# Optimization experiments

Hardware: AMD Instinct MI355X
Metric: run time of the kernel (lower is better)

The kernel has to match this reference:

```python
import jax, jax.numpy as jnp
import numpy as np

EMBED_DIM = 768
FF_DIM = 3072
NUM_EXPERTS = 8
TOP_K = 2
CAPACITY_FACTOR = 1.25  # training-mode capacity factor
LB_WEIGHT = 0.01
Z_WEIGHT = 0.001


def setup_inputs() -> dict:
    key = jax.random.key(0)
    k0, k1, k2, k3, k4 = jax.random.split(key, 5)
    B, S, D, F, E = 4, 2048, EMBED_DIM, FF_DIM, NUM_EXPERTS
    scale_d = 1.0 / np.sqrt(D)
    scale_f = 1.0 / np.sqrt(F)
    return {
        "x": jax.random.normal(k0, (B, S, D), dtype=jnp.float32),
        # router gate: nn.Linear(D, E, bias=False) -> weight [E, D]
        "w_gate": jax.random.normal(k1, (E, D), dtype=jnp.float32) * scale_d,
        # stacked expert weights, torch Linear layout [out, in]
        "wi_gate": jax.random.normal(k2, (E, F, D), dtype=jnp.float32) * scale_d,
        "wi_up": jax.random.normal(k3, (E, F, D), dtype=jnp.float32) * scale_d,
        "wo": jax.random.normal(k4, (E, D, F), dtype=jnp.float32) * scale_f,
    }


def moe_forward(x, w_gate, wi_gate, wi_up, wo):
    B, S, D = x.shape
    E = w_gate.shape[0]
    K = TOP_K
    T = B * S
    capacity = max(int(T * K / E * CAPACITY_FACTOR), K)

    xf = x.reshape(T, D)
    router_logits = xf @ w_gate.T                        # [T, E]
    router_probs = jax.nn.softmax(router_logits, axis=-1)
    topk_probs, topk_idx = jax.lax.top_k(router_probs, K)  # [T, K]
    topk_probs = topk_probs / topk_probs.sum(axis=-1, keepdims=True)

    # one-hot dispatch mask [T, K, E]
    onehot = (topk_idx[:, :, None] == jnp.arange(E)[None, None, :]).astype(xf.dtype)
    # per-(k, expert) arrival rank of each token (torch truncates first `capacity`
    # tokens in token-index order, independently per k and per expert)
    rank = ((jnp.cumsum(onehot, axis=0) - onehot) * onehot).sum(-1)  # [T, K]
    keep = (rank < capacity).astype(xf.dtype)                        # [T, K]

    # combine weights per (token, expert) [T, E]
    combine = jnp.einsum('tk,tk,tke->te', topk_probs, keep, onehot)

    out = jnp.zeros_like(xf)
    for e in range(E):  # fixed small structural loop over experts
        gate = jax.nn.silu(xf @ wi_gate[e].T)   # [T, F]
        up = xf @ wi_up[e].T                    # [T, F]
        y = (gate * up) @ wo[e].T               # [T, D]
        out = out + y * combine[:, e:e + 1]

    # auxiliary losses
    expert_mask = onehot.sum(axis=1)            # [T, E]
    f = expert_mask.sum(axis=0) / (T * K)
    P = router_probs.mean(axis=0)
    load_balance_loss = E * (f * P).sum()
    z_loss = jnp.mean(jax.nn.logsumexp(router_logits, axis=-1) ** 2)
    aux_loss = LB_WEIGHT * load_balance_loss + Z_WEIGHT * z_loss

    return out.reshape(B, S, D), aux_loss


def reference(x, w_gate, wi_gate, wi_up, wo):
    return moe_forward(x, w_gate, wi_gate, wi_up, wo)
```

## Files before the change

### kernel.cpp

```cpp
#include <hip/hip_runtime.h>

typedef unsigned short u16;
typedef unsigned int u32;
typedef unsigned long long u64;

#define T_TOK 8192
#define DIM 768
#define FF 3072
#define NE 8
#define CAP 2560
#define LSTR 5120
#define MAXMT 20

typedef __attribute__((ext_vector_type(8))) short s8v;
typedef __attribute__((ext_vector_type(4))) float f4v;

__device__ __forceinline__ u16 f2bf(float f) {
  union { float f; u32 u; } v; v.f = f;
  u32 r = v.u + 0x7FFFu + ((v.u >> 16) & 1u);
  return (u16)(r >> 16);
}

__device__ __forceinline__ void glds16(const void* g, void* l) {
  __builtin_amdgcn_global_load_lds(
      (const __attribute__((address_space(1))) u32*)g,
      (__attribute__((address_space(3))) u32*)l, 16, 0, 0);
}

__global__ void cast_bf16_kernel(const float* __restrict__ src, u16* __restrict__ dst, int n8) {
  int i = blockIdx.x * blockDim.x + threadIdx.x;
  if (i >= n8) return;
  const float4* s4 = (const float4*)src;
  float4 a = s4[2 * i], b = s4[2 * i + 1];
  uint4 o;
  o.x = (u32)f2bf(a.x) | ((u32)f2bf(a.y) << 16);
  o.y = (u32)f2bf(a.z) | ((u32)f2bf(a.w) << 16);
  o.z = (u32)f2bf(b.x) | ((u32)f2bf(b.y) << 16);
  o.w = (u32)f2bf(b.z) | ((u32)f2bf(b.w) << 16);
  ((uint4*)dst)[i] = o;
}

__global__ __launch_bounds__(256) void router_kernel(
    const float* __restrict__ x, const float* __restrict__ wg,
    int* __restrict__ tki, float* __restrict__ tkp,
    float* __restrict__ probs, float* __restrict__ lse2) {
  int lane = threadIdx.x & 63;
  int t = blockIdx.x * 4 + (threadIdx.x >> 6);
  const float* xr = x + (long)t * DIM;
  float acc[NE];
#pragma unroll
  for (int e = 0; e < NE; e++) acc[e] = 0.f;
  for (int i = 0; i < DIM / 64; i++) {
    float xv = xr[lane + 64 * i];
#pragma unroll
    for (int e = 0; e < NE; e++) acc[e] += xv * wg[e * DIM + lane + 64 * i];
  }
#pragma unroll
  for (int off = 32; off > 0; off >>= 1) {
#pragma unroll
    for (int e = 0; e < NE; e++) acc[e] += __shfl_xor(acc[e], off);
  }
  if (lane == 0) {
    float m = acc[0];
#pragma unroll
    for (int e = 1; e < NE; e++) m = fmaxf(m, acc[e]);
    float p[NE], s = 0.f;
#pragma unroll
    for (int e = 0; e < NE; e++) { p[e] = __expf(acc[e] - m); s += p[e]; }
    float inv = 1.f / s;
    int e0 = 0;
#pragma unroll
    for (int e = 1; e < NE; e++) if (acc[e] > acc[e0]) e0 = e;
    int e1 = (e0 == 0) ? 1 : 0;
#pragma unroll
    for (int e = 0; e < NE; e++) if (e != e0 && acc[e] > acc[e1]) e1 = e;
    float p0 = p[e0] * inv, p1 = p[e1] * inv;
    float rn = 1.f / (p0 + p1);
    tki[2 * t] = e0; tki[2 * t + 1] = e1;
    tkp[2 * t] = p0 * rn; tkp[2 * t + 1] = p1 * rn;
    float4 pa = {p[0] * inv, p[1] * inv, p[2] * inv, p[3] * inv};
    float4 pb = {p[4] * inv, p[5] * inv, p[6] * inv, p[7] * inv};
    ((float4*)(probs + t * 8))[0] = pa;
    ((float4*)(probs + t * 8))[1] = pb;
    float lse = __logf(s) + m;
    lse2[t] = lse * lse;
  }
}

__global__ __launch_bounds__(1024) void reduce_router_kernel(
    const int* __restrict__ tki, const float* __restrict__ probs, const float* __restrict__ lse2,
    int* __restrict__ fcnt, float* __restrict__ psum, float* __restrict__ zsum) {
  int t = blockIdx.x * 1024 + threadIdx.x;
  float4 pa = ((const float4*)(probs + t * 8))[0];
  float4 pb = ((const float4*)(probs + t * 8))[1];
  float p[8] = {pa.x, pa.y, pa.z, pa.w, pb.x, pb.y, pb.z, pb.w};
  float z = lse2[t];
  int e0 = tki[2 * t], e1 = tki[2 * t + 1];
  int fc[8];
#pragma unroll
  for (int e = 0; e < 8; e++) fc[e] = (e0 == e ? 1 : 0) + (e1 == e ? 1 : 0);
#pragma unroll
  for (int off = 32; off > 0; off >>= 1) {
#pragma unroll
    for (int e = 0; e < 8; e++) { p[e] += __shfl_xor(p[e], off); fc[e] += __shfl_xor(fc[e], off); }
    z += __shfl_xor(z, off);
  }
  __shared__ float sp[16][9];
  __shared__ int sf[16][8];
  int wv = threadIdx.x >> 6, lane = threadIdx.x & 63;
  if (lane == 0) {
#pragma unroll
    for (int e = 0; e < 8; e++) { sp[wv][e] = p[e]; sf[wv][e] = fc[e]; }
    sp[wv][8] = z;
  }
  __syncthreads();
  if (threadIdx.x < 9) {
    float s = 0.f;
    for (int w = 0; w < 16; w++) s += sp[w][threadIdx.x];
    if (threadIdx.x < 8) atomicAdd(&psum[threadIdx.x], s);
    else atomicAdd(zsum, s);
  }
  if (threadIdx.x >= 64 && threadIdx.x < 72) {
    int e = threadIdx.x - 64;
    int s = 0;
    for (int w = 0; w < 16; w++) s += sf[w][e];
    atomicAdd(&fcnt[e], s);
  }
}

__global__ __launch_bounds__(1024) void rank_dispatch_kernel(
    const int* __restrict__ tki, const float* __restrict__ tkp,
    int* __restrict__ ltk, float* __restrict__ lw,
    int* __restrict__ counts, int* __restrict__ baserow) {
  __shared__ int wave_cnt[2][16][8];
  __shared__ int base[2][8];
  __shared__ int epos[8];
  int tid = threadIdx.x, wv = tid >> 6, lane = tid & 63;
  if (tid < 16) base[tid >> 3][tid & 7] = 0;
  if (tid < 8) epos[tid] = 0;
  __syncthreads();
  u64 lmask = (lane == 63) ? 0x7FFFFFFFFFFFFFFFull : ((1ull << lane) - 1ull);
  for (int c = 0; c < T_TOK / 1024; c++) {
    int t = c * 1024 + tid;
    int e0 = tki[2 * t], e1 = tki[2 * t + 1];
    float p0 = tkp[2 * t], p1 = tkp[2 * t + 1];
    int pre0 = 0, pre1 = 0;
    for (int e = 0; e < 8; e++) {
      u64 m0 = __ballot(e0 == e);
      if (e0 == e) pre0 = __popcll(m0 & lmask);
      if (lane == 0) wave_cnt[0][wv][e] = __popcll(m0);
      u64 m1 = __ballot(e1 == e);
      if (e1 == e) pre1 = __popcll(m1 & lmask);
      if (lane == 0) wave_cnt[1][wv][e] = __popcll(m1);
    }
    __syncthreads();
    if (tid < 16) {
      int k = tid >> 3, e = tid & 7;
      int run = base[k][e];
      for (int w = 0; w < 16; w++) {
        int v = wave_cnt[k][w][e];
        wave_cnt[k][w][e] = run;
        run += v;
      }
      base[k][e] = run;
    }
    __syncthreads();
    int r0 = wave_cnt[0][wv][e0] + pre0;
    int r1 = wave_cnt[1][wv][e1] + pre1;
    if (r0 < CAP) { int p = atomicAdd(&epos[e0], 1); ltk[e0 * LSTR + p] = (t << 1); lw[e0 * LSTR + p] = p0; }
    if (r1 < CAP) { int p = atomicAdd(&epos[e1], 1); ltk[e1 * LSTR + p] = (t << 1) | 1; lw[e1 * LSTR + p] = p1; }
    __syncthreads();
  }
  if (tid == 0) {
    int run = 0;
    for (int e = 0; e < 8; e++) { counts[e] = epos[e]; baserow[e] = run; run += epos[e]; }
  }
}

__global__ __launch_bounds__(256, 2) void gemm1_kernel(
    const u16* __restrict__ xb, const u16* __restrict__ wgb, const u16* __restrict__ wub,
    u16* __restrict__ H, const int* __restrict__ counts, const int* __restrict__ baserow,
    const int* __restrict__ ltk) {
  int id = blockIdx.x;
  int xcd = id & 7;
  int q = id >> 3;
  int gg = q / MAXMT;
  int mt = q - gg * MAXMT;
  int g = gg * 8 + xcd;
  int e = g / 48;
  int nt = g - e * 48;
  int cnt = counts[e];
  if (mt * 128 >= cnt) return;

  __shared__ u16 As[128 * 32];
  __shared__ u16 Bg[64 * 32];
  __shared__ u16 Bu[64 * 32];
  __shared__ int toks[128];
  int tid = threadIdx.x;
  if (tid < 128) {
    int r = mt * 128 + tid; if (r > cnt - 1) r = cnt - 1;
    toks[tid] = ltk[e * LSTR + r] >> 1;
  }
  __syncthreads();
  int rq = tid >> 2;
  int kc = (tid & 3) * 8;
  long tA0 = toks[rq], tA1 = toks[64 + rq];
  const u16* gA0 = xb + tA0 * DIM + kc;
  const u16* gA1 = xb + tA1 * DIM + kc;
  long bOff = ((long)e * FF + nt * 64 + rq) * DIM + kc;
  const u16* gG0 = wgb + bOff;
  const u16* gU0 = wub + bOff;
  u16* dA0 = As + tid * 8; u16* dA1 = As + (256 + tid) * 8;
  u16* dG0 = Bg + tid * 8;
  u16* dU0 = Bu + tid * 8;

  int lane = tid & 63, wv = tid >> 6;
  int wm = (wv & 1) * 64, wn = (wv >> 1) * 32;
  int lrow = lane & 15, quad = lane >> 4;

  f4v zero = {0.f, 0.f, 0.f, 0.f};
  f4v accg[4][2], accu[4][2];
#pragma unroll
  for (int i = 0; i < 4; i++)
#pragma unroll
    for (int j = 0; j < 2; j++) { accg[i][j] = zero; accu[i][j] = zero; }

  for (int kt = 0; kt < DIM / 32; kt++) {
    int ko = kt * 32;
    __syncthreads();
    glds16(gA0 + ko, dA0); glds16(gA1 + ko, dA1);
    glds16(gG0 + ko, dG0);
    glds16(gU0 + ko, dU0);
    __syncthreads();
    s8v a[4], bg[2], bu[2];
#pragma unroll
    for (int i = 0; i < 4; i++)
      a[i] = *(const s8v*)&As[(wm + i * 16 + lrow) * 32 + quad * 8];
#pragma unroll
    for (int j = 0; j < 2; j++) {
      bg[j] = *(const s8v*)&Bg[(wn + j * 16 + lrow) * 32 + quad * 8];
      bu[j] = *(const s8v*)&Bu[(wn + j * 16 + lrow) * 32 + quad * 8];
    }
#pragma unroll
    for (int i = 0; i < 4; i++)
#pragma unroll
      for (int j = 0; j < 2; j++) {
        accg[i][j] = __builtin_amdgcn_mfma_f32_16x16x32_bf16(a[i], bg[j], accg[i][j], 0, 0, 0);
        accu[i][j] = __builtin_amdgcn_mfma_f32_16x16x32_bf16(a[i], bu[j], accu[i][j], 0, 0, 0);
      }
  }
  long hb = (long)baserow[e] + (long)mt * 128;
#pragma unroll
  for (int i = 0; i < 4; i++) {
#pragma unroll
    for (int r = 0; r < 4; r++) {
      int m = wm + i * 16 + quad * 4 + r;
      if (mt * 128 + m < cnt) {
#pragma unroll
        for (int j = 0; j < 2; j++) {
          float gv = accg[i][j][r], uv = accu[i][j][r];
          float h = gv / (1.f + __expf(-gv)) * uv;
          H[(hb + m) * FF + nt * 64 + wn + j * 16 + lrow] = f2bf(h);
        }
      }
    }
  }
}

__global__ __launch_bounds__(256, 2) void gemm2_kernel(
    const u16* __restrict__ H, const u16* __restrict__ wob,
    float* __restrict__ out, const int* __restrict__ counts, const int* __restrict__ baserow,
    const int* __restrict__ ltk, const float* __restrict__ lw) {
  int id = blockIdx.x;
  int xcd = id & 7;
  int q = id >> 3;
  int gg = q / 6;
  int nt = q - gg * 6;
  int g = gg * 8 + xcd;
  int e = g / MAXMT;
  int mt = g - e * MAXMT;
  int cnt = counts[e];
  if (mt * 128 >= cnt) return;

  __shared__ u16 As[128 * 32];
  __shared__ u16 Bs[128 * 32];
  __shared__ int stok[128];
  __shared__ float sw[128];
  int tid = threadIdx.x;
  if (tid < 128) {
    int r = mt * 128 + tid; if (r > cnt - 1) r = cnt - 1;
    stok[tid] = ltk[e * LSTR + r];
    sw[tid] = lw[e * LSTR + r];
  }
  long hb = (long)baserow[e] + (long)mt * 128;
  int rq = tid >> 2, kc = (tid & 3) * 8;
  const u16* gA0 = H + (hb + rq) * FF + kc;
  const u16* gA1 = gA0 + 64l * FF;
  long bOff = ((long)e * DIM + nt * 128 + rq) * FF + kc;
  const u16* gB0 = wob + bOff;
  const u16* gB1 = gB0 + 64l * FF;
  u16* dA0 = As + tid * 8; u16* dA1 = As + (256 + tid) * 8;
  u16* dB0 = Bs + tid * 8; u16* dB1 = Bs + (256 + tid) * 8;
  int lane = tid & 63, wv = tid >> 6;
  int wm = (wv & 1) * 64, wn = (wv >> 1) * 64;
  int lrow = lane & 15, quad = lane >> 4;
  f4v zero = {0.f, 0.f, 0.f, 0.f};
  f4v acc[4][4];
#pragma unroll
  for (int i = 0; i < 4; i++)
#pragma unroll
    for (int j = 0; j < 4; j++) acc[i][j] = zero;

  for (int kt = 0; kt < FF / 32; kt++) {
    int ko = kt * 32;
    __syncthreads();
    glds16(gA0 + ko, dA0); glds16(gA1 + ko, dA1);
    glds16(gB0 + ko, dB0); glds16(gB1 + ko, dB1);
    __syncthreads();
    s8v a[4], b[4];
#pragma unroll
    for (int i = 0; i < 4; i++)
      a[i] = *(const s8v*)&As[(wm + i * 16 + lrow) * 32 + quad * 8];
#pragma unroll
    for (int j = 0; j < 4; j++)
      b[j] = *(const s8v*)&Bs[(wn + j * 16 + lrow) * 32 + quad * 8];
#pragma unroll
    for (int i = 0; i < 4; i++)
#pragma unroll
      for (int j = 0; j < 4; j++)
        acc[i][j] = __builtin_amdgcn_mfma_f32_16x16x32_bf16(a[i], b[j], acc[i][j], 0, 0, 0);
  }
#pragma unroll
  for (int i = 0; i < 4; i++) {
#pragma unroll
    for (int r = 0; r < 4; r++) {
      int m = wm + i * 16 + quad * 4 + r;
      if (mt * 128 + m < cnt) {
        int entry = stok[m];
        int t = entry >> 1;
        float w = sw[m];
        long ob = (long)t * DIM + nt * 128;
#pragma unroll
        for (int j = 0; j < 4; j++)
          atomicAdd(&out[ob + wn + j * 16 + lrow], acc[i][j][r] * w);
      }
    }
  }
}

__global__ void aux_kernel(const int* __restrict__ fcnt, const float* __restrict__ psum,
                           const float* __restrict__ zsum, float* __restrict__ outaux) {
  if (threadIdx.x == 0 && blockIdx.x == 0) {
    float lb = 0.f;
    for (int e = 0; e < 8; e++)
      lb += ((float)fcnt[e] / (float)(T_TOK * 2)) * (psum[e] / (float)T_TOK);
    lb *= 8.f;
    float z = zsum[0] / (float)T_TOK;
    outaux[0] = 0.01f * lb + 0.001f * z;
  }
}

extern "C" void kernel_launch(void* const* d_in, const int* in_sizes, int n_in,
                              void* d_out, int out_size, void* d_ws, size_t ws_size,
                              hipStream_t stream) {
  const float* x = (const float*)d_in[0];
  const float* wgate = (const float*)d_in[1];
  const float* wig = (const float*)d_in[2];
  const float* wiu = (const float*)d_in[3];
  const float* wo = (const float*)d_in[4];
  float* out = (float*)d_out;

  char* ws = (char*)d_ws;
  size_t off = 0;
  auto alloc = [&](size_t bytes) {
    void* p = ws + off;
    off += (bytes + 255) & ~(size_t)255;
    return p;
  };
  int* ctrl = (int*)alloc(256);
  u16* xb = (u16*)alloc((size_t)T_TOK * DIM * 2);
  u16* wgb = (u16*)alloc((size_t)NE * FF * DIM * 2);
  u16* wub = (u16*)alloc((size_t)NE * FF * DIM * 2);
  u16* wob = (u16*)alloc((size_t)NE * DIM * FF * 2);
  u16* Hbuf = (u16*)alloc((size_t)(T_TOK * 2 + 128) * FF * 2);
  int* tki = (int*)alloc((size_t)T_TOK * 2 * 4);
  float* tkp = (float*)alloc((size_t)T_TOK * 2 * 4);
  int* ltk = (int*)alloc((size_t)NE * LSTR * 4);
  float* lw = (float*)alloc((size_t)NE * LSTR * 4);
  float* probs = (float*)alloc((size_t)T_TOK * 8 * 4);
  float* lse2 = (float*)alloc((size_t)T_TOK * 4);

  int* fcnt = ctrl;
  int* counts = ctrl + 8;
  int* baserow = ctrl + 16;
  float* psum = (float*)(ctrl + 24);
  float* zsum = (float*)(ctrl + 32);

  hipMemsetAsync(ctrl, 0, 256, stream);
  hipMemsetAsync(out, 0, (size_t)out_size * 4, stream);
  cast_bf16_kernel<<<T_TOK * DIM / 8 / 256, 256, 0, stream>>>(x, xb, T_TOK * DIM / 8);
  cast_bf16_kernel<<<NE * FF * DIM / 8 / 256, 256, 0, stream>>>(wig, wgb, NE * FF * DIM / 8);
  cast_bf16_kernel<<<NE * FF * DIM / 8 / 256, 256, 0, stream>>>(wiu, wub, NE * FF * DIM / 8);
  cast_bf16_kernel<<<NE * DIM * FF / 8 / 256, 256, 0, stream>>>(wo, wob, NE * DIM * FF / 8);
  router_kernel<<<T_TOK / 4, 256, 0, stream>>>(x, wgate, tki, tkp, probs, lse2);
  reduce_router_kernel<<<T_TOK / 1024, 1024, 0, stream>>>(tki, probs, lse2, fcnt, psum, zsum);
  rank_dispatch_kernel<<<1, 1024, 0, stream>>>(tki, tkp, ltk, lw, counts, baserow);
  gemm1_kernel<<<8 * 48 * MAXMT, 256, 0, stream>>>(xb, wgb, wub, Hbuf, counts, baserow, ltk);
  gemm2_kernel<<<8 * MAXMT * 6, 256, 0, stream>>>(Hbuf, wob, out, counts, baserow, ltk, lw);
  aux_kernel<<<1, 64, 0, stream>>>(fcnt, psum, zsum, out + (size_t)T_TOK * DIM);
}
```

Before: 646.9 us.

## Double K-tile depth to 64 and XOR-swizzle LDS layout in expert GEMMs

Result: faster. 601.7 us (-7.0%).

```diff
diff --git a/kernel.cpp b/kernel.cpp
--- a/kernel.cpp
+++ b/kernel.cpp
@@ -192,9 +192,9 @@
   int cnt = counts[e];
   if (mt * 128 >= cnt) return;
 
-  __shared__ u16 As[128 * 32];
-  __shared__ u16 Bg[64 * 32];
-  __shared__ u16 Bu[64 * 32];
+  __shared__ u16 As[128 * 64];
+  __shared__ u16 Bg[64 * 64];
+  __shared__ u16 Bu[64 * 64];
   __shared__ int toks[128];
   int tid = threadIdx.x;
   if (tid < 128) {
@@ -202,21 +202,26 @@
     toks[tid] = ltk[e * LSTR + r] >> 1;
   }
   __syncthreads();
-  int rq = tid >> 2;
-  int kc = (tid & 3) * 8;
-  long tA0 = toks[rq], tA1 = toks[64 + rq];
-  const u16* gA0 = xb + tA0 * DIM + kc;
-  const u16* gA1 = xb + tA1 * DIM + kc;
-  long bOff = ((long)e * FF + nt * 64 + rq) * DIM + kc;
-  const u16* gG0 = wgb + bOff;
-  const u16* gU0 = wub + bOff;
-  u16* dA0 = As + tid * 8; u16* dA1 = As + (256 + tid) * 8;
-  u16* dG0 = Bg + tid * 8;
-  u16* dU0 = Bu + tid * 8;
+  int rq8 = tid >> 3;
+  int swz = ((tid & 7) ^ (rq8 & 7)) * 8;
+  long tA0 = toks[rq8], tA1 = toks[32 + rq8], tA2 = toks[64 + rq8], tA3 = toks[96 + rq8];
+  const u16* gA0 = xb + tA0 * DIM + swz;
+  const u16* gA1 = xb + tA1 * DIM + swz;
+  const u16* gA2 = xb + tA2 * DIM + swz;
+  const u16* gA3 = xb + tA3 * DIM + swz;
+  long bO0 = ((long)e * FF + nt * 64 + rq8) * DIM + swz;
+  long bO1 = bO0 + 32l * DIM;
+  const u16* gG0 = wgb + bO0; const u16* gG1 = wgb + bO1;
+  const u16* gU0 = wub + bO0; const u16* gU1 = wub + bO1;
+  u16* dA0 = As + tid * 8; u16* dA1 = dA0 + 2048; u16* dA2 = dA0 + 4096; u16* dA3 = dA0 + 6144;
+  u16* dG0 = Bg + tid * 8; u16* dG1 = dG0 + 2048;
+  u16* dU0 = Bu + tid * 8; u16* dU1 = dU0 + 2048;
 
   int lane = tid & 63, wv = tid >> 6;
   int wm = (wv & 1) * 64, wn = (wv >> 1) * 32;
   int lrow = lane & 15, quad = lane >> 4;
+  int sl0 = (quad ^ (lrow & 7)) * 8;
+  int sl1 = ((quad + 4) ^ (lrow & 7)) * 8;
 
   f4v zero = {0.f, 0.f, 0.f, 0.f};
   f4v accg[4][2], accu[4][2];
@@ -225,29 +230,34 @@
 #pragma unroll
     for (int j = 0; j < 2; j++) { accg[i][j] = zero; accu[i][j] = zero; }
 
-  for (int kt = 0; kt < DIM / 32; kt++) {
-    int ko = kt * 32;
+  for (int kt = 0; kt < DIM / 64; kt++) {
+    int ko = kt * 64;
     __syncthreads();
     glds16(gA0 + ko, dA0); glds16(gA1 + ko, dA1);
-    glds16(gG0 + ko, dG0);
-    glds16(gU0 + ko, dU0);
-    __syncthreads();
-    s8v a[4], bg[2], bu[2];
-#pragma unroll
-    for (int i = 0; i < 4; i++)
-      a[i] = *(const s8v*)&As[(wm + i * 16 + lrow) * 32 + quad * 8];
-#pragma unroll
-    for (int j = 0; j < 2; j++) {
-      bg[j] = *(const s8v*)&Bg[(wn + j * 16 + lrow) * 32 + quad * 8];
-      bu[j] = *(const s8v*)&Bu[(wn + j * 16 + lrow) * 32 + quad * 8];
-    }
-#pragma unroll
-    for (int i = 0; i < 4; i++)
+    glds16(gA2 + ko, dA2); glds16(gA3 + ko, dA3);
+    glds16(gG0 + ko, dG0); glds16(gG1 + ko, dG1);
+    glds16(gU0 + ko, dU0); glds16(gU1 + ko, dU1);
+    __syncthreads();
+#pragma unroll
+    for (int kk = 0; kk < 2; kk++) {
+      int sl = kk ? sl1 : sl0;
+      s8v a[4], bgf[2], buf[2];
+#pragma unroll
+      for (int i = 0; i < 4; i++)
+        a[i] = *(const s8v*)&As[(wm + i * 16 + lrow) * 64 + sl];
 #pragma unroll
       for (int j = 0; j < 2; j++) {
-        accg[i][j] = __builtin_amdgcn_mfma_f32_16x16x32_bf16(a[i], bg[j], accg[i][j], 0, 0, 0);
-        accu[i][j] = __builtin_amdgcn_mfma_f32_16x16x32_bf16(a[i], bu[j], accu[i][j], 0, 0, 0);
+        bgf[j] = *(const s8v*)&Bg[(wn + j * 16 + lrow) * 64 + sl];
+        buf[j] = *(const s8v*)&Bu[(wn + j * 16 + lrow) * 64 + sl];
       }
+#pragma unroll
+      for (int i = 0; i < 4; i++)
+#pragma unroll
+        for (int j = 0; j < 2; j++) {
+          accg[i][j] = __builtin_amdgcn_mfma_f32_16x16x32_bf16(a[i], bgf[j], accg[i][j], 0, 0, 0);
+          accu[i][j] = __builtin_amdgcn_mfma_f32_16x16x32_bf16(a[i], buf[j], accu[i][j], 0, 0, 0);
+        }
+    }
   }
   long hb = (long)baserow[e] + (long)mt * 128;
 #pragma unroll
@@ -282,8 +292,8 @@
   int cnt = counts[e];
   if (mt * 128 >= cnt) return;
 
-  __shared__ u16 As[128 * 32];
-  __shared__ u16 Bs[128 * 32];
+  __shared__ u16 As[128 * 64];
+  __shared__ u16 Bs[128 * 64];
   __shared__ int stok[128];
   __shared__ float sw[128];
   int tid = threadIdx.x;
@@ -293,17 +303,24 @@
     sw[tid] = lw[e * LSTR + r];
   }
   long hb = (long)baserow[e] + (long)mt * 128;
-  int rq = tid >> 2, kc = (tid & 3) * 8;
-  const u16* gA0 = H + (hb + rq) * FF + kc;
-  const u16* gA1 = gA0 + 64l * FF;
-  long bOff = ((long)e * DIM + nt * 128 + rq) * FF + kc;
+  int rq8 = tid >> 3;
+  int swz = ((tid & 7) ^ (rq8 & 7)) * 8;
+  const u16* gA0 = H + (hb + rq8) * FF + swz;
+  const u16* gA1 = gA0 + 32l * FF;
+  const u16* gA2 = gA0 + 64l * FF;
+  const u16* gA3 = gA0 + 96l * FF;
+  long bOff = ((long)e * DIM + nt * 128 + rq8) * FF + swz;
   const u16* gB0 = wob + bOff;
-  const u16* gB1 = gB0 + 64l * FF;
-  u16* dA0 = As + tid * 8; u16* dA1 = As + (256 + tid) * 8;
-  u16* dB0 = Bs + tid * 8; u16* dB1 = Bs + (256 + tid) * 8;
+  const u16* gB1 = gB0 + 32l * FF;
+  const u16* gB2 = gB0 + 64l * FF;
+  const u16* gB3 = gB0 + 96l * FF;
+  u16* dA0 = As + tid * 8; u16* dA1 = dA0 + 2048; u16* dA2 = dA0 + 4096; u16* dA3 = dA0 + 6144;
+  u16* dB0 = Bs + tid * 8; u16* dB1 = dB0 + 2048; u16* dB2 = dB0 + 4096; u16* dB3 = dB0 + 6144;
   int lane = tid & 63, wv = tid >> 6;
   int wm = (wv & 1) * 64, wn = (wv >> 1) * 64;
   int lrow = lane & 15, quad = lane >> 4;
+  int sl0 = (quad ^ (lrow & 7)) * 8;
+  int sl1 = ((quad + 4) ^ (lrow & 7)) * 8;
   f4v zero = {0.f, 0.f, 0.f, 0.f};
   f4v acc[4][4];
 #pragma unroll
@@ -311,24 +328,30 @@
 #pragma unroll
     for (int j = 0; j < 4; j++) acc[i][j] = zero;
 
-  for (int kt = 0; kt < FF / 32; kt++) {
-    int ko = kt * 32;
+  for (int kt = 0; kt < FF / 64; kt++) {
+    int ko = kt * 64;
     __syncthreads();
     glds16(gA0 + ko, dA0); glds16(gA1 + ko, dA1);
+    glds16(gA2 + ko, dA2); glds16(gA3 + ko, dA3);
     glds16(gB0 + ko, dB0); glds16(gB1 + ko, dB1);
-    __syncthreads();
-    s8v a[4], b[4];
-#pragma unroll
-    for (int i = 0; i < 4; i++)
-      a[i] = *(const s8v*)&As[(wm + i * 16 + lrow) * 32 + quad * 8];
-#pragma unroll
-    for (int j = 0; j < 4; j++)
-      b[j] = *(const s8v*)&Bs[(wn + j * 16 + lrow) * 32 + quad * 8];
-#pragma unroll
-    for (int i = 0; i < 4; i++)
+    glds16(gB2 + ko, dB2); glds16(gB3 + ko, dB3);
+    __syncthreads();
+#pragma unroll
+    for (int kk = 0; kk < 2; kk++) {
+      int sl = kk ? sl1 : sl0;
+      s8v a[4], b[4];
+#pragma unroll
+      for (int i = 0; i < 4; i++)
+        a[i] = *(const s8v*)&As[(wm + i * 16 + lrow) * 64 + sl];
 #pragma unroll
       for (int j = 0; j < 4; j++)
-        acc[i][j] = __builtin_amdgcn_mfma_f32_16x16x32_bf16(a[i], b[j], acc[i][j], 0, 0, 0);
+        b[j] = *(const s8v*)&Bs[(wn + j * 16 + lrow) * 64 + sl];
+#pragma unroll
+      for (int i = 0; i < 4; i++)
+#pragma unroll
+        for (int j = 0; j < 4; j++)
+          acc[i][j] = __builtin_amdgcn_mfma_f32_16x16x32_bf16(a[i], b[j], acc[i][j], 0, 0, 0);
+    }
   }
 #pragma unroll
   for (int i = 0; i < 4; i++) {
```
